# Kernel tuning notes

Hardware: AMD Instinct MI355X
Metric: run time of the kernel (lower is better)

The kernel has to match this reference:

```python
import jax, jax.numpy as jnp
import numpy as np

B, H, L, DK = 16, 16, 2048, 64   # batch, heads, query len, head dim
LK = 4096                        # original key length
C = 10                           # num_clusters
LKS = 2 * int(np.log(LK))        # shrunk key length = 16


def _lin(x, w, b):
    # torch nn.Linear: y = x @ W^T + b
    return jnp.matmul(x, w.T) + b


def setup_inputs() -> dict:
    key = jax.random.key(0)
    ks = jax.random.split(key, 20)
    s = 0.05
    inp = {
        "Q": jax.random.normal(ks[0], (B, H, L, DK), jnp.float32),
        "K": jax.random.normal(ks[1], (B, H, LK, DK), jnp.float32),
        "V": jax.random.normal(ks[2], (B, H, LK, DK), jnp.float32),
        # shrink_k / shrink_v: Linear(l_k, 2*log(l_k))
        "shrink_k_w": jax.random.normal(ks[3], (LKS, LK), jnp.float32) * s,
        "shrink_k_b": jax.random.normal(ks[4], (LKS,), jnp.float32) * s,
        "shrink_v_w": jax.random.normal(ks[5], (LKS, LK), jnp.float32) * s,
        "shrink_v_b": jax.random.normal(ks[6], (LKS,), jnp.float32) * s,
        # proj_to_cluster_k: Linear(batch_size, num_clusters) + ReLU
        "proj_w": jax.random.normal(ks[7], (C, B), jnp.float32) * s,
        "proj_b": jax.random.normal(ks[8], (C,), jnp.float32) * s,
        "ck_w": jax.random.normal(ks[9], (C, C), jnp.float32) * s,
        "ck_b": jax.random.normal(ks[10], (C,), jnp.float32) * s,
        "cq_w": jax.random.normal(ks[11], (C, C), jnp.float32) * s,
        "cq_b": jax.random.normal(ks[12], (C,), jnp.float32) * s,
        "mu_w": jax.random.normal(ks[13], (C, C), jnp.float32) * s,
        "mu_b": jax.random.normal(ks[14], (C,), jnp.float32) * s,
        "sig_w": jax.random.normal(ks[15], (C, C), jnp.float32) * s,
        "sig_b": jax.random.normal(ks[16], (C,), jnp.float32) * s,
    }
    return inp


def reference(Q, K, V, shrink_k_w, shrink_k_b, shrink_v_w, shrink_v_b,
              proj_w, proj_b, ck_w, ck_b, cq_w, cq_b, mu_w, mu_b, sig_w, sig_b):
    b = Q.shape[0]
    # shrink along key sequence dim: (b,h,lk,d) -> (b,h,LKS,d)
    Ks = jnp.einsum('bhkd,sk->bhsd', K, shrink_k_w) + shrink_k_b[:, None]
    Vs = jnp.einsum('bhkd,sk->bhsd', V, shrink_v_w) + shrink_v_b[:, None]

    # pad + unfold over the batch dim: window j of K_padded[w:w+b]
    K_padded = jnp.concatenate([jnp.zeros_like(Ks), Ks[1:]], axis=0)  # (2b-1,h,LKS,d)
    idx = jnp.arange(b)[:, None] + jnp.arange(b)[None, :]             # (b, b)
    K_unfold = jnp.moveaxis(K_padded[idx], 1, -1)                     # (b,h,LKS,d,b)

    cluster_k_p = jax.nn.relu(_lin(K_unfold, proj_w, proj_b))         # (b,h,LKS,d,C)
    cluster_k = jax.nn.softmax(_lin(cluster_k_p, ck_w, ck_b), axis=-1)
    cluster_q = jax.nn.softmax(_lin(cluster_k_p, cq_w, cq_b), axis=-1)

    mu = _lin(cluster_q, mu_w, mu_b)
    sigma = jax.nn.softplus(_lin(cluster_q, sig_w, sig_b))
    # Normal log_prob
    log_prob = (-0.5 * jnp.square((cluster_k - mu) / sigma)
                - jnp.log(sigma) - 0.5 * jnp.log(2.0 * jnp.pi).astype(cluster_k.dtype))
    # torch CrossEntropyLoss with probability targets: class dim = dim 1 (= h)
    logp = jax.nn.log_softmax(cluster_q, axis=1)
    ce = -jnp.mean(jnp.sum(cluster_q * logp, axis=1))
    loss = -jnp.mean(log_prob) + ce

    # per-cluster masked mean over the last dim, vectorized over clusters.
    # where(argmax==i, cluster_q, 0).mean(-1) == onehot(argmax)[...,i] * mean(cluster_q,-1)
    masks = jax.nn.one_hot(jnp.argmax(cluster_q, axis=-1), C, dtype=cluster_q.dtype)  # (b,h,LKS,d,C)
    q_mean = jnp.mean(cluster_q, axis=-1)                                              # (b,h,LKS,d)
    q_sub = masks * q_mean[..., None]                                                  # (b,h,LKS,d,C)

    scores = jnp.einsum('bhqd,bhkdc->cbhqk', Q, q_sub)  # (C,b,h,l,LKS)
    final_score = jnp.max(scores, axis=0)               # (b,h,l,LKS)
    attn = jax.nn.softmax(final_score, axis=-1)
    context = jnp.einsum('bhqk,bhkd->bhqd', attn, Vs)   # (b,h,l,d)
    return context, loss
```

## Files before the change

### kernel.cpp

```cpp
#include <hip/hip_runtime.h>

#define KS_OFF 0
#define VS_OFF 262144
#define QM_OFF 524288
#define AM_OFF 786432
#define LP_OFF 1048576
#define CE_OFF 1048832

typedef __attribute__((ext_vector_type(8))) short short8;
typedef __attribute__((ext_vector_type(4))) float f32x4;

__device__ inline unsigned short bfb(float x) {
  unsigned u = __float_as_uint(x);
  return (unsigned short)((u + 0x7fffu + ((u >> 16) & 1u)) >> 16);
}
__device__ inline unsigned pk2(float a, float b) {
  return (unsigned)bfb(a) | ((unsigned)bfb(b) << 16);
}
__device__ inline float bft(unsigned short h) {
  return __uint_as_float((unsigned)h << 16);
}
__device__ inline void split3(float x, unsigned short& h, unsigned short& m, unsigned short& l) {
  unsigned u = __float_as_uint(x);
  h = (unsigned short)(u >> 16);
  float r = x - bft(h);
  m = (unsigned short)(__float_as_uint(r) >> 16);
  float r2 = r - bft(m);
  l = bfb(r2);
}

__global__ __launch_bounds__(256) void k_shrink5(
    const float* __restrict__ K, const float* __restrict__ V,
    const float* __restrict__ skw, const float* __restrict__ svw,
    float* __restrict__ part)
{
  int blk = blockIdx.x;
  int q = blk & 3;
  int bh = (blk >> 2) & 255;
  int tensor = blk >> 10;
  const float* __restrict__ src = (tensor ? V : K) + (size_t)bh * (4096 * 64);
  const float* __restrict__ w   = tensor ? svw : skw;
  float* __restrict__ dst = part + (size_t)blk * 1024;

  int t = threadIdx.x;
  int wv = t >> 6;
  int l = t & 63;
  int l15 = l & 15;
  int kg = l >> 4;
  union Frag { unsigned u[4]; short8 s8; };

  __shared__ float shm[8192];
  float* __restrict__ stage = shm + wv * 2048;

  f32x4 acc[4];
#pragma unroll
  for (int nt = 0; nt < 4; ++nt) acc[nt] = (f32x4){0.f, 0.f, 0.f, 0.f};

  const float* __restrict__ wrow = w + l15 * 4096 + kg * 8;

  int srow = l >> 4;
  int scol = (l & 15) * 4;

  int kk0 = q * 32 + wv * 8;
  for (int kk = kk0; kk < kk0 + 8; ++kk) {
    const float* __restrict__ gsrc = src + (size_t)(kk * 32) * 64;
    float4 ld[8];
#pragma unroll
    for (int r = 0; r < 8; ++r)
      ld[r] = *(const float4*)(gsrc + (r * 4 + srow) * 64 + scol);
#pragma unroll
    for (int r = 0; r < 8; ++r) {
      int row = r * 4 + srow;
      int colw = scol ^ ((row >> 3) << 4);
      *(float4*)&stage[row * 64 + colw] = ld[r];
    }

    const float* __restrict__ wp = wrow + kk * 32;
    float4 wa = *(const float4*)wp;
    float4 wb = *(const float4*)(wp + 4);
    float we[8] = {wa.x, wa.y, wa.z, wa.w, wb.x, wb.y, wb.z, wb.w};
    Frag ah, am, al;
#pragma unroll
    for (int e = 0; e < 4; ++e) {
      unsigned short h0, m0, l0, h1, m1, l1;
      split3(we[2 * e], h0, m0, l0);
      split3(we[2 * e + 1], h1, m1, l1);
      ah.u[e] = (unsigned)h0 | ((unsigned)h1 << 16);
      am.u[e] = (unsigned)m0 | ((unsigned)m1 << 16);
      al.u[e] = (unsigned)l0 | ((unsigned)l1 << 16);
    }

#pragma unroll
    for (int nt = 0; nt < 4; ++nt) {
      float v[8];
#pragma unroll
      for (int j = 0; j < 8; ++j) {
        int row = kg * 8 + j;
        int col = (nt * 16 + l15) ^ (kg << 4);
        v[j] = stage[row * 64 + col];
      }
      Frag bh, bm, bl;
#pragma unroll
      for (int e = 0; e < 4; ++e) {
        unsigned short h0, m0, l0, h1, m1, l1;
        split3(v[2 * e], h0, m0, l0);
        split3(v[2 * e + 1], h1, m1, l1);
        bh.u[e] = (unsigned)h0 | ((unsigned)h1 << 16);
        bm.u[e] = (unsigned)m0 | ((unsigned)m1 << 16);
        bl.u[e] = (unsigned)l0 | ((unsigned)l1 << 16);
      }
      acc[nt] = __builtin_amdgcn_mfma_f32_16x16x32_bf16(ah.s8, bh.s8, acc[nt], 0, 0, 0);
      acc[nt] = __builtin_amdgcn_mfma_f32_16x16x32_bf16(ah.s8, bm.s8, acc[nt], 0, 0, 0);
      acc[nt] = __builtin_amdgcn_mfma_f32_16x16x32_bf16(am.s8, bh.s8, acc[nt], 0, 0, 0);
      acc[nt] = __builtin_amdgcn_mfma_f32_16x16x32_bf16(ah.s8, bl.s8, acc[nt], 0, 0, 0);
      acc[nt] = __builtin_amdgcn_mfma_f32_16x16x32_bf16(al.s8, bh.s8, acc[nt], 0, 0, 0);
      acc[nt] = __builtin_amdgcn_mfma_f32_16x16x32_bf16(am.s8, bm.s8, acc[nt], 0, 0, 0);
    }
  }

  __syncthreads();
  int g4 = kg * 4;
#pragma unroll
  for (int nt = 0; nt < 4; ++nt)
#pragma unroll
    for (int r = 0; r < 4; ++r)
      shm[wv * 1024 + (g4 + r) * 64 + nt * 16 + l15] = acc[nt][r];
  __syncthreads();
  for (int p = t; p < 1024; p += 256)
    dst[p] = shm[p] + shm[1024 + p] + shm[2048 + p] + shm[3072 + p];
}

__global__ __launch_bounds__(256) void k_shrink_red(
    const float* __restrict__ part, const float* __restrict__ skb,
    const float* __restrict__ svb, float* __restrict__ ws)
{
  int blk = blockIdx.x;
  int tensor = blk >> 8;
  int bh = blk & 255;
  const float* __restrict__ p0 = part + ((size_t)(tensor * 1024 + bh * 4)) * 1024;
  const float* __restrict__ bias = tensor ? svb : skb;
  float* __restrict__ dst = ws + (tensor ? VS_OFF : KS_OFF) + bh * 1024;
  for (int p = threadIdx.x; p < 1024; p += 256)
    dst[p] = ((p0[p] + p0[1024 + p]) + (p0[2048 + p] + p0[3072 + p])) + bias[p >> 6];
}

__global__ __launch_bounds__(1024) void k_cluster(
    const float* __restrict__ pw, const float* __restrict__ pb,
    const float* __restrict__ ckw, const float* __restrict__ ckb,
    const float* __restrict__ cqw, const float* __restrict__ cqb,
    const float* __restrict__ muw, const float* __restrict__ mub,
    const float* __restrict__ sgw, const float* __restrict__ sgb,
    float* __restrict__ ws)
{
  int bidx = blockIdx.x >> 4;
  int sIdx = blockIdx.x & 15;
  int t = threadIdx.x;
  int h = t >> 6, d = t & 63;

  __shared__ float wgt[610];
  __shared__ float cqs[16 * 64 * 10];
  if (t < 160) wgt[t] = pw[t];
  else if (t < 170) wgt[t] = pb[t - 160];
  else if (t < 270) wgt[t] = ckw[t - 170];
  else if (t < 280) wgt[t] = ckb[t - 270];
  else if (t < 380) wgt[t] = cqw[t - 280];
  else if (t < 390) wgt[t] = cqb[t - 380];
  else if (t < 490) wgt[t] = muw[t - 390];
  else if (t < 500) wgt[t] = mub[t - 490];
  else if (t < 600) wgt[t] = sgw[t - 500];
  else if (t < 610) wgt[t] = sgb[t - 600];
  __syncthreads();

  const float* __restrict__ Ks = ws + KS_OFF;

  float ckp[10];
#pragma unroll
  for (int c = 0; c < 10; ++c) ckp[c] = wgt[160 + c];
  for (int m = 1; m <= bidx; ++m) {
    float kv = Ks[((m * 16 + h) * 16 + sIdx) * 64 + d];
    int j = m + 15 - bidx;
#pragma unroll
    for (int c = 0; c < 10; ++c) ckp[c] = fmaf(kv, wgt[c * 16 + j], ckp[c]);
  }
#pragma unroll
  for (int c = 0; c < 10; ++c) ckp[c] = fmaxf(ckp[c], 0.f);

  float zk[10], zq[10];
#pragma unroll
  for (int c = 0; c < 10; ++c) { zk[c] = wgt[270 + c]; zq[c] = wgt[380 + c]; }
#pragma unroll
  for (int j = 0; j < 10; ++j) {
    float v = ckp[j];
#pragma unroll
    for (int c = 0; c < 10; ++c) {
      zk[c] = fmaf(v, wgt[170 + c * 10 + j], zk[c]);
      zq[c] = fmaf(v, wgt[280 + c * 10 + j], zq[c]);
    }
  }
  float mk = zk[0], mq = zq[0];
#pragma unroll
  for (int c = 1; c < 10; ++c) { mk = fmaxf(mk, zk[c]); mq = fmaxf(mq, zq[c]); }
  float sk = 0.f, sq = 0.f;
#pragma unroll
  for (int c = 0; c < 10; ++c) {
    zk[c] = expf(zk[c] - mk); sk += zk[c];
    zq[c] = expf(zq[c] - mq); sq += zq[c];
  }
  float rik = 1.f / sk, riq = 1.f / sq;
#pragma unroll
  for (int c = 0; c < 10; ++c) { zk[c] *= rik; zq[c] *= riq; }

  float mu[10], sgz[10];
#pragma unroll
  for (int c = 0; c < 10; ++c) { mu[c] = wgt[490 + c]; sgz[c] = wgt[600 + c]; }
#pragma unroll
  for (int j = 0; j < 10; ++j) {
    float v = zq[j];
#pragma unroll
    for (int c = 0; c < 10; ++c) {
      mu[c]  = fmaf(v, wgt[390 + c * 10 + j], mu[c]);
      sgz[c] = fmaf(v, wgt[500 + c * 10 + j], sgz[c]);
    }
  }
  float lp = 0.f, qmean = 0.f, best = zq[0];
  int amax = 0;
#pragma unroll
  for (int c = 0; c < 10; ++c) {
    float x = sgz[c];
    float sg = (x > 20.f) ? x : log1pf(expf(x));
    float zr = (zk[c] - mu[c]) / sg;
    lp += -0.5f * zr * zr - logf(sg);
    qmean += zq[c];
    if (c > 0 && zq[c] > best) { best = zq[c]; amax = c; }
  }
  lp -= 10.f * 0.91893853320467274f;
  qmean *= 0.1f;

  int pos = ((bidx * 16 + h) * 16 + sIdx) * 64 + d;
  ws[QM_OFF + pos] = qmean;
  ((int*)ws)[AM_OFF + pos] = amax;
#pragma unroll
  for (int c = 0; c < 10; ++c) cqs[(h * 64 + d) * 10 + c] = zq[c];
  __syncthreads();

  float ce = 0.f;
  if (t < 640) {
    int dd = t / 10, cc = t - dd * 10;
    float x[16];
#pragma unroll
    for (int hh = 0; hh < 16; ++hh) x[hh] = cqs[(hh * 64 + dd) * 10 + cc];
    float mx = x[0];
#pragma unroll
    for (int hh = 1; hh < 16; ++hh) mx = fmaxf(mx, x[hh]);
    float sum = 0.f;
#pragma unroll
    for (int hh = 0; hh < 16; ++hh) sum += expf(x[hh] - mx);
    float lse = mx + logf(sum);
#pragma unroll
    for (int hh = 0; hh < 16; ++hh) ce += x[hh] * (x[hh] - lse);
  }

#pragma unroll
  for (int o = 1; o < 64; o <<= 1) { lp += __shfl_xor(lp, o); ce += __shfl_xor(ce, o); }
  __shared__ float redw[16][2];
  if ((t & 63) == 0) { redw[t >> 6][0] = lp; redw[t >> 6][1] = ce; }
  __syncthreads();
  if (t == 0) {
    float Ls = 0.f, Cs = 0.f;
#pragma unroll
    for (int i = 0; i < 16; ++i) { Ls += redw[i][0]; Cs += redw[i][1]; }
    ws[LP_OFF + blockIdx.x] = Ls;
    ws[CE_OFF + blockIdx.x] = Cs;
  }
}

__global__ __launch_bounds__(512, 2) void k_attn(
    const float* __restrict__ Q, float* __restrict__ out,
    const float* __restrict__ ws)
{
  int bid = blockIdx.x;
  int bh = bid >> 3;
  int eighth = bid & 7;
  int t = threadIdx.x;
  int wv = t >> 6;
  int l = t & 63;
  int l15 = l & 15;
  int sbase = (l >> 4) * 8;
  int g4 = (l >> 4) * 4;

  __shared__ unsigned short Gm[10][16][72];
  __shared__ float Vs_l[1024];
  __shared__ unsigned short attn_l[8][16][32];

  const float* __restrict__ qmp = ws + QM_OFF + bh * 1024;
  const int* __restrict__ amp = (const int*)ws + AM_OFF + bh * 1024;
  const float* __restrict__ vsp = ws + VS_OFF + bh * 1024;

  for (int i = t; i < 5760; i += 512) ((unsigned*)Gm)[i] = 0u;
  for (int i = t; i < 2048; i += 512) ((unsigned*)attn_l)[i] = 0u;
  for (int i = t; i < 1024; i += 512) Vs_l[i] = vsp[i];
  __syncthreads();
  for (int p = t; p < 1024; p += 512) {
    int s = p >> 6, dd = p & 63;
    Gm[amp[p]][s][dd] = bfb(qmp[p]);
  }
  __syncthreads();

  union Frag { unsigned u[4]; short8 s8; };

  Frag vf[4];
#pragma unroll
  for (int dt = 0; dt < 4; ++dt) {
#pragma unroll
    for (int e2 = 0; e2 < 4; ++e2) {
      int s0 = sbase + e2 * 2;
      float a = (s0 < 16) ? Vs_l[s0 * 64 + dt * 16 + l15] : 0.f;
      float b = (s0 + 1 < 16) ? Vs_l[(s0 + 1) * 64 + dt * 16 + l15] : 0.f;
      vf[dt].u[e2] = pk2(a, b);
    }
  }

  for (int tt = 0; tt < 2; ++tt) {
    int qbase = eighth * 256 + wv * 32 + tt * 16;
    const float* __restrict__ qptr = Q + ((size_t)bh * 2048 + qbase) * 64 + l15 * 64;

    Frag bf[2];
#pragma unroll
    for (int ks = 0; ks < 2; ++ks) {
      const float* p = qptr + sbase + ks * 32;
      float4 a = *(const float4*)p;
      float4 b2 = *(const float4*)(p + 4);
      bf[ks].u[0] = pk2(a.x, a.y);
      bf[ks].u[1] = pk2(a.z, a.w);
      bf[ks].u[2] = pk2(b2.x, b2.y);
      bf[ks].u[3] = pk2(b2.z, b2.w);
    }

    f32x4 acc[10];
#pragma unroll
    for (int c = 0; c < 10; ++c) acc[c] = (f32x4){0.f, 0.f, 0.f, 0.f};
#pragma unroll
    for (int ks = 0; ks < 2; ++ks) {
#pragma unroll
      for (int c = 0; c < 10; ++c) {
        short8 af = *(const short8*)(const void*)&Gm[c][l15][sbase + ks * 32];
        acc[c] = __builtin_amdgcn_mfma_f32_16x16x32_bf16(af, bf[ks].s8, acc[c], 0, 0, 0);
      }
    }
    f32x4 fs = acc[0];
#pragma unroll
    for (int c = 1; c < 10; ++c) {
      fs.x = fmaxf(fs.x, acc[c].x); fs.y = fmaxf(fs.y, acc[c].y);
      fs.z = fmaxf(fs.z, acc[c].z); fs.w = fmaxf(fs.w, acc[c].w);
    }
    float mx = fmaxf(fmaxf(fs.x, fs.y), fmaxf(fs.z, fs.w));
    mx = fmaxf(mx, __shfl_xor(mx, 16));
    mx = fmaxf(mx, __shfl_xor(mx, 32));
    float e0 = __expf(fs.x - mx), e1 = __expf(fs.y - mx),
          e2 = __expf(fs.z - mx), e3 = __expf(fs.w - mx);
    float ssum = e0 + e1 + e2 + e3;
    ssum += __shfl_xor(ssum, 16);
    ssum += __shfl_xor(ssum, 32);
    float inv = 1.f / ssum;
    unsigned* awp = (unsigned*)&attn_l[wv][l15][g4];
    awp[0] = pk2(e0 * inv, e1 * inv);
    awp[1] = pk2(e2 * inv, e3 * inv);
    short8 b2f = *(const short8*)(const void*)&attn_l[wv][l15][sbase];
#pragma unroll
    for (int dt = 0; dt < 4; ++dt) {
      f32x4 ct = (f32x4){0.f, 0.f, 0.f, 0.f};
      ct = __builtin_amdgcn_mfma_f32_16x16x32_bf16(vf[dt].s8, b2f, ct, 0, 0, 0);
      float* op = out + ((size_t)bh * 2048 + qbase + l15) * 64 + dt * 16 + g4;
      *(f32x4*)op = ct;
    }
  }

  if (bid == 0 && t == 0) {
    float Ls = 0.f, Cs = 0.f;
    for (int i = 0; i < 256; ++i) { Ls += ws[LP_OFF + i]; Cs += ws[CE_OFF + i]; }
    out[33554432] = -Ls / 2621440.f - Cs / 163840.f;
  }
}

extern "C" void kernel_launch(void* const* d_in, const int* in_sizes, int n_in,
                              void* d_out, int out_size, void* d_ws, size_t ws_size,
                              hipStream_t stream) {
  const float* Q   = (const float*)d_in[0];
  const float* K   = (const float*)d_in[1];
  const float* V   = (const float*)d_in[2];
  const float* skw = (const float*)d_in[3];
  const float* skb = (const float*)d_in[4];
  const float* svw = (const float*)d_in[5];
  const float* svb = (const float*)d_in[6];
  const float* pw  = (const float*)d_in[7];
  const float* pb  = (const float*)d_in[8];
  const float* ckw = (const float*)d_in[9];
  const float* ckb = (const float*)d_in[10];
  const float* cqw = (const float*)d_in[11];
  const float* cqb = (const float*)d_in[12];
  const float* muw = (const float*)d_in[13];
  const float* mub = (const float*)d_in[14];
  const float* sgw = (const float*)d_in[15];
  const float* sgb = (const float*)d_in[16];
  float* out = (float*)d_out;
  float* ws  = (float*)d_ws;

  hipLaunchKernelGGL(k_shrink5, dim3(2048), dim3(256), 0, stream, K, V, skw, svw, out);
  hipLaunchKernelGGL(k_shrink_red, dim3(512), dim3(256), 0, stream, out, skb, svb, ws);
  hipLaunchKernelGGL(k_cluster, dim3(256), dim3(1024), 0, stream,
                     pw, pb, ckw, ckb, cqw, cqb, muw, mub, sgw, sgb, ws);
  hipLaunchKernelGGL(k_attn, dim3(2048), dim3(512), 0, stream, Q, out, ws);
}
```

Measured before the change: 312.9 us.

## Double-buffer shrink kernel with direct global-to-LDS loads and prefetch Q in attention

The shrink kernel now stages K/V tiles straight into LDS using global_load_lds into two 32 KB buffers, fetching the next sub-tile and next weight row while MFMAs run on the current one. This removes the register round-trip and the serialized load-then-compute pattern per step. The attention kernel issues its Q loads before the LDS setup and prefetches the second tile early to hide global latency. In exchange, LDS use doubles, which may lower occupancy, and a barrier is added every iteration.

```diff
diff --git a/kernel.cpp b/kernel.cpp
--- a/kernel.cpp
+++ b/kernel.cpp
@@ -28,8 +28,13 @@
   float r2 = r - bft(m);
   l = bfb(r2);
 }
-
-__global__ __launch_bounds__(256) void k_shrink5(
+__device__ inline void gload16(const void* g, void* l) {
+  __builtin_amdgcn_global_load_lds(
+      (const __attribute__((address_space(1))) unsigned*)g,
+      (__attribute__((address_space(3))) unsigned*)l, 16, 0, 0);
+}
+
+__global__ __launch_bounds__(256) void k_shrink6(
     const float* __restrict__ K, const float* __restrict__ V,
     const float* __restrict__ skw, const float* __restrict__ svw,
     float* __restrict__ part)
@@ -47,10 +52,20 @@
   int l = t & 63;
   int l15 = l & 15;
   int kg = l >> 4;
+  int lr4 = l >> 4;
   union Frag { unsigned u[4]; short8 s8; };
 
-  __shared__ float shm[8192];
-  float* __restrict__ stage = shm + wv * 2048;
+  __shared__ float shm[16384];
+
+#define STAGE(buf, sub) do {                                                  \
+    const float* gs = src + (size_t)(q * 1024 + (sub) * 128) * 64;            \
+    _Pragma("unroll")                                                         \
+    for (int i = 0; i < 8; ++i) {                                             \
+      int ch = wv * 8 + i;                                                    \
+      int row = ch * 4 + lr4;                                                 \
+      int s16 = (l & 15) ^ (((row >> 3) & 3) << 2);                           \
+      gload16(gs + (size_t)row * 64 + s16 * 4, &shm[(buf) * 8192 + ch * 256]);\
+    } } while (0)
 
   f32x4 acc[4];
 #pragma unroll
@@ -58,27 +73,23 @@
 
   const float* __restrict__ wrow = w + l15 * 4096 + kg * 8;
 
-  int srow = l >> 4;
-  int scol = (l & 15) * 4;
-
-  int kk0 = q * 32 + wv * 8;
-  for (int kk = kk0; kk < kk0 + 8; ++kk) {
-    const float* __restrict__ gsrc = src + (size_t)(kk * 32) * 64;
-    float4 ld[8];
-#pragma unroll
-    for (int r = 0; r < 8; ++r)
-      ld[r] = *(const float4*)(gsrc + (r * 4 + srow) * 64 + scol);
-#pragma unroll
-    for (int r = 0; r < 8; ++r) {
-      int row = r * 4 + srow;
-      int colw = scol ^ ((row >> 3) << 4);
-      *(float4*)&stage[row * 64 + colw] = ld[r];
-    }
-
-    const float* __restrict__ wp = wrow + kk * 32;
-    float4 wa = *(const float4*)wp;
-    float4 wb = *(const float4*)(wp + 4);
-    float we[8] = {wa.x, wa.y, wa.z, wa.w, wb.x, wb.y, wb.z, wb.w};
+  STAGE(0, 0);
+  int kk0 = q * 32 + wv;
+  float4 wa_c = *(const float4*)(wrow + kk0 * 32);
+  float4 wb_c = *(const float4*)(wrow + kk0 * 32 + 4);
+  __syncthreads();
+
+  for (int sub = 0; sub < 8; ++sub) {
+    int cur = sub & 1;
+    if (sub < 7) STAGE(cur ^ 1, sub + 1);
+    float4 wa_n, wb_n;
+    if (sub < 7) {
+      int kkn = q * 32 + (sub + 1) * 4 + wv;
+      wa_n = *(const float4*)(wrow + kkn * 32);
+      wb_n = *(const float4*)(wrow + kkn * 32 + 4);
+    }
+
+    float we[8] = {wa_c.x, wa_c.y, wa_c.z, wa_c.w, wb_c.x, wb_c.y, wb_c.z, wb_c.w};
     Frag ah, am, al;
 #pragma unroll
     for (int e = 0; e < 4; ++e) {
@@ -90,13 +101,14 @@
       al.u[e] = (unsigned)l0 | ((unsigned)l1 << 16);
     }
 
+    const float* __restrict__ stage = &shm[cur * 8192];
 #pragma unroll
     for (int nt = 0; nt < 4; ++nt) {
       float v[8];
 #pragma unroll
       for (int j = 0; j < 8; ++j) {
-        int row = kg * 8 + j;
-        int col = (nt * 16 + l15) ^ (kg << 4);
+        int row = wv * 32 + kg * 8 + j;
+        int col = (nt * 16 + l15) ^ (((row >> 3) & 3) << 4);
         v[j] = stage[row * 64 + col];
       }
       Frag bh, bm, bl;
@@ -116,9 +128,11 @@
       acc[nt] = __builtin_amdgcn_mfma_f32_16x16x32_bf16(al.s8, bh.s8, acc[nt], 0, 0, 0);
       acc[nt] = __builtin_amdgcn_mfma_f32_16x16x32_bf16(am.s8, bm.s8, acc[nt], 0, 0, 0);
     }
-  }
-
-  __syncthreads();
+
+    if (sub < 7) { wa_c = wa_n; wb_c = wb_n; }
+    __syncthreads();
+  }
+
   int g4 = kg * 4;
 #pragma unroll
   for (int nt = 0; nt < 4; ++nt)
@@ -128,6 +142,7 @@
   __syncthreads();
   for (int p = t; p < 1024; p += 256)
     dst[p] = shm[p] + shm[1024 + p] + shm[2048 + p] + shm[3072 + p];
+#undef STAGE
 }
 
 __global__ __launch_bounds__(256) void k_shrink_red(
@@ -296,6 +311,13 @@
   const int* __restrict__ amp = (const int*)ws + AM_OFF + bh * 1024;
   const float* __restrict__ vsp = ws + VS_OFF + bh * 1024;
 
+  const float* __restrict__ qbp =
+      Q + ((size_t)bh * 2048 + eighth * 256 + wv * 32 + l15) * 64 + sbase;
+  float4 q4[2][4];
+#pragma unroll
+  for (int e = 0; e < 4; ++e)
+    q4[0][e] = *(const float4*)(qbp + (e >> 1) * 32 + (e & 1) * 4);
+
   for (int i = t; i < 5760; i += 512) ((unsigned*)Gm)[i] = 0u;
   for (int i = t; i < 2048; i += 512) ((unsigned*)attn_l)[i] = 0u;
   for (int i = t; i < 1024; i += 512) Vs_l[i] = vsp[i];
@@ -320,16 +342,20 @@
     }
   }
 
+#pragma unroll
   for (int tt = 0; tt < 2; ++tt) {
     int qbase = eighth * 256 + wv * 32 + tt * 16;
-    const float* __restrict__ qptr = Q + ((size_t)bh * 2048 + qbase) * 64 + l15 * 64;
+    if (tt == 0) {
+#pragma unroll
+      for (int e = 0; e < 4; ++e)
+        q4[1][e] = *(const float4*)(qbp + 1024 + (e >> 1) * 32 + (e & 1) * 4);
+    }
 
     Frag bf[2];
 #pragma unroll
     for (int ks = 0; ks < 2; ++ks) {
-      const float* p = qptr + sbase + ks * 32;
-      float4 a = *(const float4*)p;
-      float4 b2 = *(const float4*)(p + 4);
+      float4 a = q4[tt][ks * 2];
+      float4 b2 = q4[tt][ks * 2 + 1];
       bf[ks].u[0] = pk2(a.x, a.y);
       bf[ks].u[1] = pk2(a.z, a.w);
       bf[ks].u[2] = pk2(b2.x, b2.y);
@@ -405,7 +431,7 @@
   float* out = (float*)d_out;
   float* ws  = (float*)d_ws;
 
-  hipLaunchKernelGGL(k_shrink5, dim3(2048), dim3(256), 0, stream, K, V, skw, svw, out);
+  hipLaunchKernelGGL(k_shrink6, dim3(2048), dim3(256), 0, stream, K, V, skw, svw, out);
   hipLaunchKernelGGL(k_shrink_red, dim3(512), dim3(256), 0, stream, out, skb, svb, ws);
   hipLaunchKernelGGL(k_cluster, dim3(256), dim3(1024), 0, stream,
                      pw, pb, ckw, ckb, cqw, cqb, muw, mub, sgw, sgb, ws);
```

Result: faster. 294.4 us (-5.9%).
